# Kernel optimization log

Hardware: AMD Instinct MI355X
Metric: run time of the kernel (lower is better)

The kernel has to match this reference:

```python
import jax, jax.numpy as jnp
import numpy as np
from jax import lax

BIG = 1e6      # 'infinite' 1D distance when no background pixel seen yet
CHUNK = 32     # column-chunk size for the parabola-min pass


def _dist_1d_along_h(mask):
    """1D distance (in pixels) along axis H to nearest False pixel.
    mask: bool [B, H, W] -> float32 [B, H, W]."""
    m = jnp.swapaxes(mask, 0, 1)  # [H, B, W], scan over H
    init = jnp.full(m.shape[1:], BIG, dtype=jnp.float32)

    def step(d, row):
        d2 = jnp.where(row, d + 1.0, 0.0)
        return d2, d2

    _, fw = lax.scan(step, init, m)
    _, bw = lax.scan(step, init, m[::-1])
    d = jnp.minimum(fw, bw[::-1])  # [H, B, W]
    return jnp.swapaxes(d, 0, 1)


def _edt(mask):
    """Exact 2D Euclidean distance transform (scipy distance_transform_edt):
    distance of each True pixel to the nearest False pixel. mask: bool [B,H,W]."""
    B, H, W = mask.shape
    g = _dist_1d_along_h(mask)          # [B, H, W] vertical 1D distances
    gsq = g * g
    nc = W // CHUNK
    j = jnp.arange(W, dtype=jnp.float32)                     # output columns
    kpos = jnp.arange(W, dtype=jnp.float32).reshape(nc, CHUNK)
    chunks = jnp.transpose(gsq.reshape(B, H, nc, CHUNK), (2, 0, 1, 3))  # [nc,B,H,K]

    def step(best, xs):
        gk, kp = xs                                          # [B,H,K], [K]
        sq = (j[:, None] - kp[None, :]) ** 2                 # [W, K]
        cand = jnp.min(gk[:, :, None, :] + sq[None, None, :, :], axis=-1)  # [B,H,W]
        return jnp.minimum(best, cand), None

    best0 = jnp.full((B, H, W), BIG * BIG, dtype=jnp.float32)
    dt_sq, _ = lax.scan(step, best0, (chunks, kpos))
    return jnp.sqrt(dt_sq)


def _dtm01(mask):
    """compute_dtm01: per-batch EDT normalized by its max; zeros if mask empty."""
    dist = _edt(mask)                                        # [B,H,W]
    any_fg = jnp.any(mask, axis=(1, 2))                      # [B]
    mx = jnp.max(dist, axis=(1, 2))                          # [B]
    mx_safe = jnp.where(mx > 0, mx, 1.0)
    return jnp.where(any_fg[:, None, None], dist / mx_safe[:, None, None], 0.0)


def reference(output, target):
    # apply_nonlin is None -> identity
    gt = target[:, 0, :, :].astype(jnp.float32)              # [B,H,W]
    gt_mask = target[:, 0, :, :] > 0                         # bool mask (astype(bool))
    seg_mask = output[:, 1, :, :] > 0.5

    gt_dtm = _dtm01(gt_mask)                                 # channel-1 DTM
    seg_dtm = _dtm01(seg_mask)

    delta_s = (output[:, 1, :, :] - gt) ** 2
    dtm = seg_dtm ** 2 + gt_dtm ** 2
    return jnp.mean(delta_s * dtm)


def setup_inputs() -> dict:
    key = jax.random.key(0)
    k1, k2 = jax.random.split(key)
    output = jax.random.normal(k1, (8, 2, 512, 512), dtype=jnp.float32)
    target = jax.random.randint(k2, (8, 1, 512, 512), 0, 2, dtype=jnp.int32)
    return {"output": output, "target": target}
```

## Files before the change

kernel.cpp:

```cpp
#include <hip/hip_runtime.h>

#define B 8
#define H 512
#define W 512
#define HW (H * W)
#define BHW (B * H * W)


__global__ __launch_bounds__(512) void vert_kernel(
    const float* __restrict__ output, const int* __restrict__ target,
    unsigned short* __restrict__ ud_gt, unsigned short* __restrict__ ud_seg,
    unsigned int* __restrict__ hdr) {
  const int tid = threadIdx.x;
  const int bx = blockIdx.x;
  if (bx == 0 && tid < 64) hdr[tid] = 0u;

  const int strip = bx & 15;
  const int b = (bx >> 4) & 7;
  const int maskSel = bx >> 7;
  const int c = tid & 31;
  const int col = strip * 32 + c;
  const int seg = tid >> 5;
  const int h0 = seg * 32;

  const int* tsrc = target + (size_t)b * HW + col;
  const float* osrc = output + (size_t)(2 * b + 1) * HW + col;
  unsigned short* dst = (maskSel ? ud_seg : ud_gt) + (size_t)b * HW + col;

  unsigned int bits = 0;
  if (maskSel == 0) {
#pragma unroll
    for (int i = 0; i < 32; ++i) {
      if (!(tsrc[(h0 + i) * W] > 0)) bits |= 1u << i;
    }
  } else {
#pragma unroll
    for (int i = 0; i < 32; ++i) {
      if (!(osrc[(h0 + i) * W] > 0.5f)) bits |= 1u << i;
    }
  }

  __shared__ int sLast[16][32];
  __shared__ int sFirst[16][32];
  sLast[seg][c] = bits ? (h0 + 31 - __clz(bits)) : -1000001;
  sFirst[seg][c] = bits ? (h0 + __ffs(bits) - 1) : 2000000;
  __syncthreads();

  int inLF = -1000001;
  int inNF = 2000000;
#pragma unroll
  for (int s = 0; s < 16; ++s) {
    int sl = sLast[s][c];
    int sf = sFirst[s][c];
    if (s < seg) inLF = max(inLF, sl);
    if (s > seg) inNF = min(inNF, sf);
  }

#pragma unroll
  for (int i = 0; i < 32; ++i) {
    const int h = h0 + i;
    unsigned int below = bits & (0xFFFFFFFFu >> (31 - i));
    unsigned int above = bits >> i;
    int lf = below ? (h0 + 31 - __clz(below)) : inLF;
    int nf = above ? (h + __ffs(above) - 1) : inNF;
    int v = min(min(h - lf, nf - h), 65535);
    dst[h * W] = (unsigned short)v;
  }
}

__global__ __launch_bounds__(512) void horiz_kernel(
    const float* __restrict__ output, const int* __restrict__ target,
    const unsigned short* __restrict__ ud_gt,
    const unsigned short* __restrict__ ud_seg, double* __restrict__ sums,
    unsigned int* __restrict__ maxbuf, unsigned int* __restrict__ counter,
    float* __restrict__ out) {
  const int tid = threadIdx.x;
  const int lane = tid & 63;
  const int wave = tid >> 6;
  const int rb = blockIdx.x * 8 + wave;
  const int b = rb >> 9;
  const int h = rb & (H - 1);

  __shared__ float sg[8][W];
  __shared__ float ss[8][W];

  const unsigned short* gRow = ud_gt + (size_t)rb * W;
  const unsigned short* sRow = ud_seg + (size_t)rb * W;
  uint4 gu = ((const uint4*)gRow)[lane];
  uint4 su = ((const uint4*)sRow)[lane];

  auto sq2 = [](unsigned int u, float& a, float& bq) {
    float x = (float)(u & 0xffffu);
    float y = (float)(u >> 16);
    a = x * x;
    bq = y * y;
  };
  float4 lo, hi;
  sq2(gu.x, lo.x, lo.y); sq2(gu.y, lo.z, lo.w);
  sq2(gu.z, hi.x, hi.y); sq2(gu.w, hi.z, hi.w);
  ((float4*)sg[wave])[2 * lane] = lo;
  ((float4*)sg[wave])[2 * lane + 1] = hi;
  sq2(su.x, lo.x, lo.y); sq2(su.y, lo.z, lo.w);
  sq2(su.z, hi.x, hi.y); sq2(su.w, hi.z, hi.w);
  ((float4*)ss[wave])[2 * lane] = lo;
  ((float4*)ss[wave])[2 * lane + 1] = hi;
  __syncthreads();

  const float* g = sg[wave];
  const float* s = ss[wave];
  float bg[8], bs[8];
  float m = 0.f;
#pragma unroll
  for (int i = 0; i < 8; ++i) {
    int j = lane + 64 * i;
    bg[i] = g[j];
    bs[i] = s[j];
    m = fmaxf(m, fmaxf(bg[i], bs[i]));
  }
  for (int r = 1; r < W; ++r) {
    float rr = (float)(r * r);
    if (rr >= m) break;
    m = 0.f;
#pragma unroll
    for (int i = 0; i < 8; ++i) {
      int j = lane + 64 * i;
      int kl = j - r, kr = j + r;
      float gl = (kl >= 0) ? g[kl] : 4e12f;
      float gr = (kr < W) ? g[kr] : 4e12f;
      float sl = (kl >= 0) ? s[kl] : 4e12f;
      float sr = (kr < W) ? s[kr] : 4e12f;
      bg[i] = fminf(bg[i], fminf(gl + rr, gr + rr));
      bs[i] = fminf(bs[i], fminf(sl + rr, sr + rr));
      m = fmaxf(m, fmaxf(bg[i], bs[i]));
    }
  }

  const float* oRow = output + (size_t)(2 * b + 1) * HW + (size_t)h * W;
  const int* tRow = target + (size_t)b * HW + (size_t)h * W;
  float mg = 0.f, ms = 0.f, sgf = 0.f, ssf = 0.f;
#pragma unroll
  for (int i = 0; i < 8; ++i) {
    int j = lane + 64 * i;
    float o = oRow[j];
    float t = (float)tRow[j];
    float dq = (o - t) * (o - t);
    sgf += dq * bg[i];
    ssf += dq * bs[i];
    mg = fmaxf(mg, bg[i]);
    ms = fmaxf(ms, bs[i]);
  }
  double sgd = (double)sgf, ssd = (double)ssf;
#pragma unroll
  for (int off = 32; off; off >>= 1) {
    sgd += __shfl_down(sgd, off);
    ssd += __shfl_down(ssd, off);
    mg = fmaxf(mg, __shfl_down(mg, off));
    ms = fmaxf(ms, __shfl_down(ms, off));
  }
  __shared__ double bsg[8], bss[8];
  __shared__ float bmg[8], bms[8];
  __shared__ unsigned int lastFlag;
  if (lane == 0) {
    bsg[wave] = sgd;
    bss[wave] = ssd;
    bmg[wave] = mg;
    bms[wave] = ms;
  }
  __syncthreads();
  if (tid == 0) {
    double tg = 0.0, ts = 0.0;
    float xg = 0.f, xs = 0.f;
#pragma unroll
    for (int wv = 0; wv < 8; ++wv) {
      tg += bsg[wv];
      ts += bss[wv];
      xg = fmaxf(xg, bmg[wv]);
      xs = fmaxf(xs, bms[wv]);
    }
    atomicAdd(&sums[b], tg);
    atomicAdd(&sums[8 + b], ts);
    atomicMax(&maxbuf[b], __float_as_uint(xg));
    atomicMax(&maxbuf[8 + b], __float_as_uint(xs));
    __threadfence();
    unsigned int old = atomicAdd(counter, 1u);
    lastFlag = (old == (unsigned int)(B * H / 8 - 1)) ? 1u : 0u;
  }
  __syncthreads();

  if (lastFlag && tid < 64) {
    __threadfence();
    double t = 0.0;
    if (tid < 8) {
      double sgv = atomicAdd(&sums[tid], 0.0);
      double ssv = atomicAdd(&sums[8 + tid], 0.0);
      float xg = __uint_as_float(atomicMax(&maxbuf[tid], 0u));
      float xs = __uint_as_float(atomicMax(&maxbuf[8 + tid], 0u));
      t = sgv / (double)(xg > 0.f ? xg : 1.f) +
          ssv / (double)(xs > 0.f ? xs : 1.f);
    }
    t += __shfl_down(t, 4);
    t += __shfl_down(t, 2);
    t += __shfl_down(t, 1);
    if (tid == 0) out[0] = (float)(t * (1.0 / (double)BHW));
  }
}

extern "C" void kernel_launch(void* const* d_in, const int* in_sizes, int n_in,
                              void* d_out, int out_size, void* d_ws,
                              size_t ws_size, hipStream_t stream) {
  const float* output = (const float*)d_in[0];
  const int* target = (const int*)d_in[1];

  double* sums = (double*)d_ws;
  unsigned int* maxbuf = (unsigned int*)((char*)d_ws + 128);
  unsigned int* counter = (unsigned int*)((char*)d_ws + 192);
  unsigned int* hdr = (unsigned int*)d_ws;
  unsigned short* ud_gt = (unsigned short*)((char*)d_ws + 256);
  unsigned short* ud_seg = ud_gt + BHW;

  vert_kernel<<<dim3(256), 512, 0, stream>>>(output, target, ud_gt, ud_seg,
                                             hdr);
  horiz_kernel<<<dim3(B * H / 8), 512, 0, stream>>>(
      output, target, ud_gt, ud_seg, sums, maxbuf, counter, (float*)d_out);
}
```

Measured before the change: 93.48 us.

## Fuse vertical and horizontal EDT passes into one cooperative kernel with grid sync

Merges the vertical distance pass and the horizontal parabola/reduction pass into a single cooperative kernel of 256 blocks separated by a grid-wide sync. This removes one kernel launch and its inter-kernel gap. Each block now handles 16 rows in the second phase instead of 8, which halves the block count for the horizontal pass. The grid sync adds a barrier cost, and the two kernels remain as a fallback if the cooperative launch fails.

```diff
diff --git a/kernel.cpp b/kernel.cpp
--- a/kernel.cpp
+++ b/kernel.cpp
@@ -1,4 +1,7 @@
 #include <hip/hip_runtime.h>
+#include <hip/hip_cooperative_groups.h>
+
+namespace cg = cooperative_groups;
 
 #define B 8
 #define H 512
@@ -6,6 +9,218 @@
 #define HW (H * W)
 #define BHW (B * H * W)
 
+
+__global__ __launch_bounds__(512) void fused_kernel(
+    const float* __restrict__ output, const int* __restrict__ target,
+    unsigned short* __restrict__ ud_gt, unsigned short* __restrict__ ud_seg,
+    unsigned int* __restrict__ hdr, double* __restrict__ sums,
+    unsigned int* __restrict__ maxbuf, unsigned int* __restrict__ counter,
+    float* __restrict__ out) {
+  const int tid = threadIdx.x;
+  const int bx = blockIdx.x;
+
+  __shared__ union {
+    struct { int last[16][32]; int first[16][32]; } v;
+    struct { float g[8][W]; float s[8][W]; } h2;
+  } sm;
+
+  if (bx == 0 && tid < 64) atomicExch(&hdr[tid], 0u);
+
+  {
+    const int g = bx & 15;
+    const int strip = bx >> 4;
+    const int b = g & 7;
+    const int maskSel = g >> 3;
+    const int c = tid & 31;
+    const int col = strip * 32 + c;
+    const int seg = tid >> 5;
+    const int h0 = seg * 32;
+
+    const int* tsrc = target + (size_t)b * HW + col;
+    const float* osrc = output + (size_t)(2 * b + 1) * HW + col;
+    unsigned short* dst = (maskSel ? ud_seg : ud_gt) + (size_t)b * HW + col;
+
+    unsigned int bits = 0;
+    if (maskSel == 0) {
+#pragma unroll
+      for (int i = 0; i < 32; ++i) {
+        if (!(tsrc[(h0 + i) * W] > 0)) bits |= 1u << i;
+      }
+    } else {
+#pragma unroll
+      for (int i = 0; i < 32; ++i) {
+        if (!(osrc[(h0 + i) * W] > 0.5f)) bits |= 1u << i;
+      }
+    }
+
+    sm.v.last[seg][c] = bits ? (h0 + 31 - __clz(bits)) : -1000001;
+    sm.v.first[seg][c] = bits ? (h0 + __ffs(bits) - 1) : 2000000;
+    __syncthreads();
+
+    int inLF = -1000001;
+    int inNF = 2000000;
+#pragma unroll
+    for (int s = 0; s < 16; ++s) {
+      int sl = sm.v.last[s][c];
+      int sf = sm.v.first[s][c];
+      if (s < seg) inLF = max(inLF, sl);
+      if (s > seg) inNF = min(inNF, sf);
+    }
+
+#pragma unroll
+    for (int i = 0; i < 32; ++i) {
+      const int h = h0 + i;
+      unsigned int below = bits & (0xFFFFFFFFu >> (31 - i));
+      unsigned int above = bits >> i;
+      int lf = below ? (h0 + 31 - __clz(below)) : inLF;
+      int nf = above ? (h + __ffs(above) - 1) : inNF;
+      int v = min(min(h - lf, nf - h), 65535);
+      dst[h * W] = (unsigned short)v;
+    }
+  }
+
+  __threadfence();
+  cg::this_grid().sync();
+  __threadfence();
+
+  const int lane = tid & 63;
+  const int wave = tid >> 6;
+  const int bb = bx & 7;
+  const int blk = bx >> 3;
+
+  float* sgw = sm.h2.g[wave];
+  float* ssw = sm.h2.s[wave];
+
+  auto sq2 = [](unsigned int u, float& a, float& bq) {
+    float x = (float)(u & 0xffffu);
+    float y = (float)(u >> 16);
+    a = x * x;
+    bq = y * y;
+  };
+
+  double sgd = 0.0, ssd = 0.0;
+  float mgAll = 0.f, msAll = 0.f;
+
+  for (int half = 0; half < 2; ++half) {
+    const int rb = bb * H + blk * 16 + half * 8 + wave;
+    const int h = rb & (H - 1);
+
+    const unsigned short* gRow = ud_gt + (size_t)rb * W;
+    const unsigned short* sRow = ud_seg + (size_t)rb * W;
+    uint4 gu = ((const uint4*)gRow)[lane];
+    uint4 su = ((const uint4*)sRow)[lane];
+
+    float4 lo, hi;
+    sq2(gu.x, lo.x, lo.y); sq2(gu.y, lo.z, lo.w);
+    sq2(gu.z, hi.x, hi.y); sq2(gu.w, hi.z, hi.w);
+    ((float4*)sgw)[2 * lane] = lo;
+    ((float4*)sgw)[2 * lane + 1] = hi;
+    sq2(su.x, lo.x, lo.y); sq2(su.y, lo.z, lo.w);
+    sq2(su.z, hi.x, hi.y); sq2(su.w, hi.z, hi.w);
+    ((float4*)ssw)[2 * lane] = lo;
+    ((float4*)ssw)[2 * lane + 1] = hi;
+
+    float bg[8], bs[8];
+    float m = 0.f;
+#pragma unroll
+    for (int i = 0; i < 8; ++i) {
+      int j = lane + 64 * i;
+      bg[i] = sgw[j];
+      bs[i] = ssw[j];
+      m = fmaxf(m, fmaxf(bg[i], bs[i]));
+    }
+    for (int r = 1; r < W; ++r) {
+      float rr = (float)(r * r);
+      if (rr >= m) break;
+      m = 0.f;
+#pragma unroll
+      for (int i = 0; i < 8; ++i) {
+        int j = lane + 64 * i;
+        int kl = j - r, kr = j + r;
+        float gl = (kl >= 0) ? sgw[kl] : 4e12f;
+        float gr = (kr < W) ? sgw[kr] : 4e12f;
+        float sl = (kl >= 0) ? ssw[kl] : 4e12f;
+        float sr = (kr < W) ? ssw[kr] : 4e12f;
+        bg[i] = fminf(bg[i], fminf(gl + rr, gr + rr));
+        bs[i] = fminf(bs[i], fminf(sl + rr, sr + rr));
+        m = fmaxf(m, fmaxf(bg[i], bs[i]));
+      }
+    }
+
+    const float* oRow = output + (size_t)(2 * bb + 1) * HW + (size_t)h * W;
+    const int* tRow = target + (size_t)bb * HW + (size_t)h * W;
+    float sgf = 0.f, ssf = 0.f, mg = 0.f, ms = 0.f;
+#pragma unroll
+    for (int i = 0; i < 8; ++i) {
+      int j = lane + 64 * i;
+      float o = oRow[j];
+      float t = (float)tRow[j];
+      float dq = (o - t) * (o - t);
+      sgf += dq * bg[i];
+      ssf += dq * bs[i];
+      mg = fmaxf(mg, bg[i]);
+      ms = fmaxf(ms, bs[i]);
+    }
+    sgd += (double)sgf;
+    ssd += (double)ssf;
+    mgAll = fmaxf(mgAll, mg);
+    msAll = fmaxf(msAll, ms);
+  }
+
+#pragma unroll
+  for (int off = 32; off; off >>= 1) {
+    sgd += __shfl_down(sgd, off);
+    ssd += __shfl_down(ssd, off);
+    mgAll = fmaxf(mgAll, __shfl_down(mgAll, off));
+    msAll = fmaxf(msAll, __shfl_down(msAll, off));
+  }
+  __shared__ double bsg[8], bss[8];
+  __shared__ float bmg[8], bms[8];
+  __shared__ unsigned int lastFlag;
+  if (lane == 0) {
+    bsg[wave] = sgd;
+    bss[wave] = ssd;
+    bmg[wave] = mgAll;
+    bms[wave] = msAll;
+  }
+  __syncthreads();
+  if (tid == 0) {
+    double tg = 0.0, ts = 0.0;
+    float xg = 0.f, xs = 0.f;
+#pragma unroll
+    for (int wv = 0; wv < 8; ++wv) {
+      tg += bsg[wv];
+      ts += bss[wv];
+      xg = fmaxf(xg, bmg[wv]);
+      xs = fmaxf(xs, bms[wv]);
+    }
+    atomicAdd(&sums[bb], tg);
+    atomicAdd(&sums[8 + bb], ts);
+    atomicMax(&maxbuf[bb], __float_as_uint(xg));
+    atomicMax(&maxbuf[8 + bb], __float_as_uint(xs));
+    __threadfence();
+    unsigned int old = atomicAdd(counter, 1u);
+    lastFlag = (old == 255u) ? 1u : 0u;
+  }
+  __syncthreads();
+
+  if (lastFlag && tid < 64) {
+    __threadfence();
+    double t = 0.0;
+    if (tid < 8) {
+      double sgv = atomicAdd(&sums[tid], 0.0);
+      double ssv = atomicAdd(&sums[8 + tid], 0.0);
+      float xg = __uint_as_float(atomicMax(&maxbuf[tid], 0u));
+      float xs = __uint_as_float(atomicMax(&maxbuf[8 + tid], 0u));
+      t = sgv / (double)(xg > 0.f ? xg : 1.f) +
+          ssv / (double)(xs > 0.f ? xs : 1.f);
+    }
+    t += __shfl_down(t, 4);
+    t += __shfl_down(t, 2);
+    t += __shfl_down(t, 1);
+    if (tid == 0) out[0] = (float)(t * (1.0 / (double)BHW));
+  }
+}
 
 __global__ __launch_bounds__(512) void vert_kernel(
     const float* __restrict__ output, const int* __restrict__ target,
@@ -217,9 +432,17 @@
   unsigned int* hdr = (unsigned int*)d_ws;
   unsigned short* ud_gt = (unsigned short*)((char*)d_ws + 256);
   unsigned short* ud_seg = ud_gt + BHW;
-
-  vert_kernel<<<dim3(256), 512, 0, stream>>>(output, target, ud_gt, ud_seg,
-                                             hdr);
-  horiz_kernel<<<dim3(B * H / 8), 512, 0, stream>>>(
-      output, target, ud_gt, ud_seg, sums, maxbuf, counter, (float*)d_out);
+  float* outp = (float*)d_out;
+
+  void* args[] = {&output, &target, &ud_gt, &ud_seg, &hdr,
+                  &sums,   &maxbuf, &counter, &outp};
+  hipError_t err = hipLaunchCooperativeKernel(
+      reinterpret_cast<void*>(fused_kernel), dim3(256), dim3(512), args, 0,
+      stream);
+  if (err != hipSuccess) {
+    vert_kernel<<<dim3(256), 512, 0, stream>>>(output, target, ud_gt, ud_seg,
+                                               hdr);
+    horiz_kernel<<<dim3(B * H / 8), 512, 0, stream>>>(
+        output, target, ud_gt, ud_seg, sums, maxbuf, counter, outp);
+  }
 }
```

New measurement: 197.5 us. +111.3%, slower.
